# Kernel tuning notes

Hardware: AMD Instinct MI355X
Metric: run time of the kernel (lower is better)

## Reference

```python
import jax, jax.numpy as jnp
import numpy as np

N = 100000; R2 = 500; H = 200; T = 3; E = 300000; R2E = 400000
SE = 4000; SR = 8; S2E = 8000
SLOPE = (1.0 / 8 + 1.0 / 3) / 2  # eval-mode F.rrelu negative slope


def l2norm(x):
    # F.normalize(x) along dim=1 with eps=1e-12
    return x / jnp.maximum(jnp.linalg.norm(x, axis=-1, keepdims=True), 1e-12)


def rrelu(x):
    return jnp.where(x >= 0, x, x * SLOPE)


def seg_mean(vals, seg, num):
    # mean of vals rows grouped by seg id; absent groups stay zero (matches x_input init)
    s = jax.ops.segment_sum(vals, seg, num_segments=num)
    c = jax.ops.segment_sum(jnp.ones((vals.shape[0],), vals.dtype), seg, num_segments=num)
    return s / jnp.maximum(c, 1.0)[:, None]


def lstm_cell(x, h, c, Wih, Whh, bih, bhh):
    g = x @ Wih.T + bih + h @ Whh.T + bhh
    i, f, gg, o = jnp.split(g, 4, axis=1)
    c2 = jax.nn.sigmoid(f) * c + jax.nn.sigmoid(i) * jnp.tanh(gg)
    return jax.nn.sigmoid(o) * jnp.tanh(c2), c2


def gru_cell(x, h, Wih, Whh, bih, bhh):
    gi = x @ Wih.T + bih
    gh = h @ Whh.T + bhh
    ir, iz, inn = jnp.split(gi, 3, axis=1)
    hr, hz, hn = jnp.split(gh, 3, axis=1)
    r = jax.nn.sigmoid(ir + hr)
    z = jax.nn.sigmoid(iz + hz)
    n = jnp.tanh(inn + r * hn)
    return (1 - z) * n + z * h


def rgcn_layer(h, rel_emb, src, dst, et, Wn, Wloop, Wevolve, num_nodes):
    # UnionRGCNLayer: msg = (h_src + rel_emb[etype]) @ W_neighbor, sum-aggregated at dst;
    # self loop uses evolve weight for nodes with in-edges, plain loop weight otherwise.
    msg = (h[src] + rel_emb[et]) @ Wn
    agg = jax.ops.segment_sum(msg, dst, num_segments=num_nodes)
    indeg = jax.ops.segment_sum(jnp.ones((src.shape[0],), h.dtype), dst, num_segments=num_nodes)
    loop = jnp.where((indeg > 0)[:, None], h @ Wevolve, h @ Wloop)
    return rrelu(agg + loop)


def setup_inputs() -> dict:
    key = jax.random.key(0)
    ks = iter(jax.random.split(key, 48))
    s = 1.0 / np.sqrt(H)
    d = {}
    d['src'] = jax.random.randint(next(ks), (T, E), 0, N)
    d['dst'] = jax.random.randint(next(ks), (T, E), 0, N)
    d['etype'] = jax.random.randint(next(ks), (T, E), 0, R2)
    d['r_to_e'] = jax.random.randint(next(ks), (T, R2E), 0, N)
    d['r_seg'] = jax.random.randint(next(ks), (T, R2E), 0, R2)
    d['s_src'] = jax.random.randint(next(ks), (T, SE), 0, R2)
    d['s_dst'] = jax.random.randint(next(ks), (T, SE), 0, R2)
    d['s_etype'] = jax.random.randint(next(ks), (T, SE), 0, SR)
    d['s_r_to_e'] = jax.random.randint(next(ks), (T, S2E), 0, R2)
    d['s_r_seg'] = jax.random.randint(next(ks), (T, S2E), 0, SR)
    d['dynamic_emb'] = jax.random.normal(next(ks), (N, H), jnp.float32)
    d['emb_rel'] = jax.random.normal(next(ks), (R2, H), jnp.float32) * s
    d['p_rel'] = jax.random.normal(next(ks), (SR, H), jnp.float32) * s
    d['Wih1'] = jax.random.normal(next(ks), (4 * H, 2 * H), jnp.float32) * s
    d['Whh1'] = jax.random.normal(next(ks), (4 * H, H), jnp.float32) * s
    d['bih1'] = jax.random.normal(next(ks), (4 * H,), jnp.float32) * s
    d['bhh1'] = jax.random.normal(next(ks), (4 * H,), jnp.float32) * s
    d['Wih2'] = jax.random.normal(next(ks), (4 * H, 2 * H), jnp.float32) * s
    d['Whh2'] = jax.random.normal(next(ks), (4 * H, H), jnp.float32) * s
    d['bih2'] = jax.random.normal(next(ks), (4 * H,), jnp.float32) * s
    d['bhh2'] = jax.random.normal(next(ks), (4 * H,), jnp.float32) * s
    d['Wih3'] = jax.random.normal(next(ks), (3 * H, H), jnp.float32) * s
    d['Whh3'] = jax.random.normal(next(ks), (3 * H, H), jnp.float32) * s
    d['bih3'] = jax.random.normal(next(ks), (3 * H,), jnp.float32) * s
    d['bhh3'] = jax.random.normal(next(ks), (3 * H,), jnp.float32) * s
    d['Wihe'] = jax.random.normal(next(ks), (3 * H, H), jnp.float32) * s
    d['Whhe'] = jax.random.normal(next(ks), (3 * H, H), jnp.float32) * s
    d['bihe'] = jax.random.normal(next(ks), (3 * H,), jnp.float32) * s
    d['bhhe'] = jax.random.normal(next(ks), (3 * H,), jnp.float32) * s
    for nm in ('Wn', 'Wl', 'We', 'sWn', 'sWl', 'sWe'):
        d[nm] = jax.random.normal(next(ks), (2, H, H), jnp.float32) * s
    return d


def reference(src, dst, etype, r_to_e, r_seg, s_src, s_dst, s_etype, s_r_to_e, s_r_seg,
              dynamic_emb, emb_rel, p_rel,
              Wih1, Whh1, bih1, bhh1, Wih2, Whh2, bih2, bhh2,
              Wih3, Whh3, bih3, bhh3, Wihe, Whhe, bihe, bhhe,
              Wn, Wl, We, sWn, sWl, sWe):
    h = l2norm(dynamic_emb)  # layer_norm=True path
    h_0 = c_0 = p_h_0 = p_c_0 = None
    history_embs = []
    rel_embs = []
    for t in range(T):
        # per-relation mean of involved entity embeddings (r_to_e grouped by uniq_r)
        x_input = seg_mean(h[r_to_e[t]], r_seg[t], R2)
        if t == 0:
            h_prev, c_prev = emb_rel, x_input
        else:
            h_prev, c_prev = h_0, c_0
        x_cat = jnp.concatenate([emb_rel, x_input], axis=1)
        h_0, c_0 = lstm_cell(x_cat, h_prev, c_prev, Wih1, Whh1, bih1, bhh1)
        h_0 = l2norm(h_0); c_0 = l2norm(c_0)
        # super-graph: per-super-relation mean of relation embeddings
        sx = seg_mean(h_0[s_r_to_e[t]], s_r_seg[t], SR)
        if t == 0:
            ph_prev, pc_prev = p_rel, sx
        else:
            ph_prev, pc_prev = p_h_0, p_c_0
        sx_cat = jnp.concatenate([p_rel, sx], axis=1)
        p_h_0, p_c_0 = lstm_cell(sx_cat, ph_prev, pc_prev, Wih2, Whh2, bih2, bhh2)
        p_h_0 = l2norm(p_h_0); p_c_0 = l2norm(p_c_0)
        # super RGCN over relation-nodes (2 UnionRGCN layers, same rel emb per layer)
        cur = h_0
        for l in range(2):
            cur = rgcn_layer(cur, p_h_0, s_src[t], s_dst[t], s_etype[t], sWn[l], sWl[l], sWe[l], R2)
        cur = l2norm(cur)
        h_0 = gru_cell(cur, h_0, Wih3, Whh3, bih3, bhh3)
        h_0 = l2norm(h_0)
        rel_embs.append(h_0)
        # entity RGCN over the snapshot graph
        cur_h = h
        for l in range(2):
            cur_h = rgcn_layer(cur_h, h_0, src[t], dst[t], etype[t], Wn[l], Wl[l], We[l], N)
        cur_h = l2norm(cur_h)
        h = gru_cell(cur_h, h, Wihe, Whhe, bihe, bhhe)
        h = l2norm(h)
        history_embs.append(h)
    return jnp.stack(history_embs), jnp.stack(rel_embs)
```

## Files before the change

kernel.cpp:

```cpp
#include <hip/hip_runtime.h>
#include <math.h>

#define N_NODES 100000
#define H 200
#define R2 500
#define T_STEPS 3
#define E_EDGES 300000
#define R2E 400000
#define SE_EDGES 4000
#define SR 8
#define S2E 8000
#define SLOPE 0.22916666666666666f
#define NB 64
#define RCHUNK ((R2E + NB - 1) / NB)
#define NCH 128
#define CHSZ ((N_NODES + NCH - 1) / NCH)
#define SPT  ((CHSZ + 255) / 256)

typedef unsigned short u16;
typedef unsigned int u32;
typedef __bf16 bf8 __attribute__((ext_vector_type(8)));
typedef float f32x4 __attribute__((ext_vector_type(4)));

static __device__ __forceinline__ float sigf(float x) { return 1.f / (1.f + expf(-x)); }
static __device__ __forceinline__ float bf2f(u32 lo16) {
    u32 v = lo16 << 16; float f; __builtin_memcpy(&f, &v, 4); return f;
}
static __device__ __forceinline__ u16 f2bf(float a) {
    __bf16 x = (__bf16)a; u16 u; __builtin_memcpy(&u, &x, 2); return u;
}
static __device__ __forceinline__ u32 pk2(float a, float b) {
    return (u32)f2bf(a) | ((u32)f2bf(b) << 16);
}
static __device__ __forceinline__ int xcd_swz(int b, int nwg) {
    int q = nwg >> 3, r = nwg & 7;
    int xcd = b & 7, u = b >> 3;
    int start = xcd * q + (xcd < r ? xcd : r);
    return start + u;
}

__global__ __launch_bounds__(256) void l2norm_k(const float* __restrict__ src, float* __restrict__ dst,
                                                u16* __restrict__ mir, int rows) {
    int wave = threadIdx.x >> 6, lane = threadIdx.x & 63;
    int r = blockIdx.x * 4 + wave;
    if (r >= rows) return;
    float4 v = make_float4(0.f, 0.f, 0.f, 0.f);
    if (lane < 50) v = *(const float4*)(src + (size_t)r * H + lane * 4);
    float s = v.x * v.x + v.y * v.y + v.z * v.z + v.w * v.w;
    for (int o = 32; o > 0; o >>= 1) s += __shfl_down(s, o);
    float rn = 1.f / fmaxf(sqrtf(__shfl(s, 0)), 1e-12f);
    if (lane < 50) {
        float4 o4 = make_float4(v.x * rn, v.y * rn, v.z * rn, v.w * rn);
        *(float4*)(dst + (size_t)r * H + lane * 4) = o4;
        if (mir) {
            uint2 u; u.x = pk2(o4.x, o4.y); u.y = pk2(o4.z, o4.w);
            *(uint2*)(mir + (size_t)r * H + lane * 4) = u;
        }
    }
}

__global__ __launch_bounds__(256) void l2norm_b_k(u16* __restrict__ buf, int rows) {
    int wave = threadIdx.x >> 6, lane = threadIdx.x & 63;
    int r = blockIdx.x * 4 + wave;
    if (r >= rows) return;
    uint2 u = make_uint2(0, 0);
    if (lane < 50) u = *(const uint2*)(buf + (size_t)r * H + lane * 4);
    float x0 = bf2f(u.x & 0xffff), x1 = bf2f(u.x >> 16);
    float x2 = bf2f(u.y & 0xffff), x3 = bf2f(u.y >> 16);
    float s = x0 * x0 + x1 * x1 + x2 * x2 + x3 * x3;
    for (int o = 32; o > 0; o >>= 1) s += __shfl_down(s, o);
    float rn = 1.f / fmaxf(sqrtf(__shfl(s, 0)), 1e-12f);
    if (lane < 50) {
        uint2 o2; o2.x = pk2(x0 * rn, x1 * rn); o2.y = pk2(x2 * rn, x3 * rn);
        *(uint2*)(buf + (size_t)r * H + lane * 4) = o2;
    }
}

__global__ void wconv4_k(const float* __restrict__ W0, const float* __restrict__ W1,
                         const float* __restrict__ W2, const float* __restrict__ W3,
                         u16* __restrict__ o) {
    int m = blockIdx.y;
    const float* W = (m == 0) ? W0 : (m == 1) ? W1 : (m == 2) ? W2 : W3;
    int i = blockIdx.x * 256 + threadIdx.x;
    if (i < 40000) { int n = i / 200, k = i - n * 200; o[m * 40000 + i] = f2bf(W[k * 200 + n]); }
}
__global__ void wconv2_k(const float* __restrict__ Wa, const float* __restrict__ Wb, u16* __restrict__ o) {
    int i = blockIdx.x * 256 + threadIdx.x;
    if (i < 240000) o[i] = f2bf(i < 120000 ? Wa[i] : Wb[i - 120000]);
}

__global__ void cnt3_k(const int* __restrict__ d, int total, int per_t, int stride, int* __restrict__ cnt) {
    int i = blockIdx.x * 256 + threadIdx.x;
    if (i < total) { int t = i / per_t; atomicAdd(&cnt[t * stride + d[i]], 1); }
}

__global__ __launch_bounds__(256) void seg_cnt3_k(const int* __restrict__ seg, int per_t, int nseg,
                                                  int blocks_per_t, int* __restrict__ cnt) {
    __shared__ int lc[500];
    int t = blockIdx.x / blocks_per_t;
    int pb = blockIdx.x - t * blocks_per_t;
    const int* s = seg + (size_t)t * per_t;
    int* c = cnt + (size_t)t * nseg;
    for (int i = threadIdx.x; i < nseg; i += 256) lc[i] = 0;
    __syncthreads();
    int chunk = (per_t + blocks_per_t - 1) / blocks_per_t;
    int beg = pb * chunk;
    int end = beg + chunk; if (end > per_t) end = per_t;
    for (int i = beg + threadIdx.x; i < end; i += 256) atomicAdd(&lc[s[i]], 1);
    __syncthreads();
    for (int i = threadIdx.x; i < nseg; i += 256) if (lc[i]) atomicAdd(&c[i], lc[i]);
}

__global__ __launch_bounds__(256) void hist3_k(const int* __restrict__ seg,
                                               int* __restrict__ hist, int* __restrict__ cnt) {
    __shared__ int lc[R2];
    int t = blockIdx.x / NB;
    int pb = blockIdx.x - t * NB;
    const int* s = seg + (size_t)t * R2E;
    for (int i = threadIdx.x; i < R2; i += 256) lc[i] = 0;
    __syncthreads();
    int beg = pb * RCHUNK;
    int end = beg + RCHUNK; if (end > R2E) end = R2E;
    for (int i = beg + threadIdx.x; i < end; i += 256) atomicAdd(&lc[s[i]], 1);
    __syncthreads();
    int* hrow = hist + (size_t)(t * NB + pb) * R2;
    int* c = cnt + (size_t)t * R2;
    for (int i = threadIdx.x; i < R2; i += 256) {
        hrow[i] = lc[i];
        if (lc[i]) atomicAdd(&c[i], lc[i]);
    }
}

__global__ __launch_bounds__(1024) void scan3_k(const int* __restrict__ cntA, int* __restrict__ offA,
                                                int* __restrict__ curA, int n) {
    const int b = blockIdx.x;
    const int* cnt = cntA + (size_t)b * n;
    int* off = offA + (size_t)b * (n + 1);
    int* cur = curA + (size_t)b * n;
    __shared__ int part[1024];
    int tid = threadIdx.x;
    int per = (n + 1023) / 1024;
    int s0 = tid * per;
    int e0 = s0 + per; if (e0 > n) e0 = n;
    int sum = 0;
    for (int i = s0; i < e0; ++i) sum += cnt[i];
    part[tid] = sum;
    __syncthreads();
    for (int d = 1; d < 1024; d <<= 1) {
        int v = (tid >= d) ? part[tid - d] : 0;
        __syncthreads();
        part[tid] += v;
        __syncthreads();
    }
    int excl = (tid == 0) ? 0 : part[tid - 1];
    for (int i = s0; i < e0; ++i) { off[i] = excl; cur[i] = excl; excl += cnt[i]; }
    if (tid == 1023) off[n] = excl;
}

__global__ __launch_bounds__(256) void scanA_k(const int* __restrict__ cntA, int* __restrict__ bsum, int n) {
    int b = blockIdx.x;
    int t = b / NCH, ch = b - t * NCH;
    const int* cnt = cntA + (size_t)t * n;
    int base = ch * CHSZ;
    int cend = base + CHSZ; if (cend > n) cend = n;
    int s0 = base + threadIdx.x * SPT;
    int e0 = s0 + SPT; if (e0 > cend) e0 = cend;
    int sum = 0;
    for (int i = s0; i < e0 && i < cend; ++i) sum += cnt[i];
    __shared__ int red[256];
    red[threadIdx.x] = (s0 < cend) ? sum : 0;
    __syncthreads();
    for (int o = 128; o > 0; o >>= 1) {
        if (threadIdx.x < o) red[threadIdx.x] += red[threadIdx.x + o];
        __syncthreads();
    }
    if (threadIdx.x == 0) bsum[t * NCH + ch] = red[0];
}

__global__ __launch_bounds__(128) void scanB_k(const int* __restrict__ bsum, int* __restrict__ boff,
                                               int* __restrict__ offA, int n) {
    int t = blockIdx.x;
    int tid = threadIdx.x;
    __shared__ int part[128];
    int v = bsum[t * NCH + tid];
    part[tid] = v;
    __syncthreads();
    for (int d = 1; d < 128; d <<= 1) {
        int u = (tid >= d) ? part[tid - d] : 0;
        __syncthreads();
        part[tid] += u;
        __syncthreads();
    }
    boff[t * NCH + tid] = part[tid] - v;
    if (tid == 127) offA[(size_t)t * (n + 1) + n] = part[127];
}

__global__ __launch_bounds__(256) void scanC_k(const int* __restrict__ cntA, const int* __restrict__ boff,
                                               int* __restrict__ offA, int* __restrict__ curA, int n) {
    int b = blockIdx.x;
    int t = b / NCH, ch = b - t * NCH;
    const int* cnt = cntA + (size_t)t * n;
    int* off = offA + (size_t)t * (n + 1);
    int* cur = curA + (size_t)t * n;
    int base = ch * CHSZ;
    int cend = base + CHSZ; if (cend > n) cend = n;
    int s0 = base + threadIdx.x * SPT;
    int e0 = s0 + SPT; if (e0 > cend) e0 = cend;
    int sum = 0;
    for (int i = s0; i < e0 && i < cend; ++i) sum += cnt[i];
    __shared__ int part[256];
    int my = (s0 < cend) ? sum : 0;
    part[threadIdx.x] = my;
    __syncthreads();
    for (int d = 1; d < 256; d <<= 1) {
        int u = (threadIdx.x >= d) ? part[threadIdx.x - d] : 0;
        __syncthreads();
        part[threadIdx.x] += u;
        __syncthreads();
    }
    int excl = boff[t * NCH + ch] + part[threadIdx.x] - my;
    for (int i = s0; i < e0 && i < cend; ++i) {
        off[i] = excl; cur[i] = excl; excl += cnt[i];
    }
}

__global__ __launch_bounds__(64) void offs3_k(const int* __restrict__ hist, const int* __restrict__ csr,
                                              int* __restrict__ offb) {
    int b = blockIdx.x;
    int t = b / R2, s = b - t * R2;
    int lane = threadIdx.x;
    int v = hist[(size_t)(t * NB + lane) * R2 + s];
    int pre = v;
    for (int o = 1; o < 64; o <<= 1) {
        int u = __shfl_up(pre, o);
        if (lane >= o) pre += u;
    }
    int base = csr[(size_t)t * (R2 + 1) + s];
    offb[(size_t)(t * NB + lane) * R2 + s] = base + pre - v;
}

__global__ __launch_bounds__(256) void part3_k(const int* __restrict__ seg, const int* __restrict__ val,
                                               const int* __restrict__ offb, int* __restrict__ outp) {
    __shared__ int cur[R2];
    int t = blockIdx.x / NB;
    int pb = blockIdx.x - t * NB;
    const int* s = seg + (size_t)t * R2E;
    const int* v = val + (size_t)t * R2E;
    const int* ob = offb + (size_t)(t * NB + pb) * R2;
    int* o = outp + (size_t)t * R2E;
    for (int i = threadIdx.x; i < R2; i += 256) cur[i] = ob[i];
    __syncthreads();
    int beg = pb * RCHUNK;
    int end = beg + RCHUNK; if (end > R2E) end = R2E;
    for (int i = beg + threadIdx.x; i < end; i += 256) {
        int p = atomicAdd(&cur[s[i]], 1);
        o[p] = v[i];
    }
}

__global__ void scatter3_k(const int* __restrict__ dst, const int* __restrict__ src,
                           const int* __restrict__ et, int* __restrict__ cur,
                           int* __restrict__ psrc, int* __restrict__ pet,
                           int per_t, int stride, int total) {
    int i = blockIdx.x * 256 + threadIdx.x;
    if (i < total) {
        int t = i / per_t;
        int p = atomicAdd(&cur[t * stride + dst[i]], 1);
        psrc[(size_t)t * per_t + p] = src[i];
        pet[(size_t)t * per_t + p] = et[i];
    }
}
__global__ void zlist3_k(const int* __restrict__ cnt, int* __restrict__ zl, int* __restrict__ nz,
                         int n, int total) {
    int i = blockIdx.x * 256 + threadIdx.x;
    if (i < total && cnt[i] == 0) {
        int t = i / n;
        int p = atomicAdd(&nz[t], 1);
        zl[(size_t)t * n + p] = i - t * n;
    }
}

#define SEG_CW 25
__global__ __launch_bounds__(256) void seg_acc_k(const float* __restrict__ hsrc,
                                                 const int* __restrict__ idx,
                                                 const int* __restrict__ seg, int n,
                                                 float* __restrict__ acc, int nseg) {
    __shared__ float lacc[500 * SEG_CW];
    int cg = blockIdx.x & 7;
    int pb = blockIdx.x >> 3;
    int NPB = gridDim.x >> 3;
    int t = threadIdx.x;
    for (int i = t; i < nseg * SEG_CW; i += 256) lacc[i] = 0.f;
    __syncthreads();
    int chunk = (n + NPB - 1) / NPB;
    int beg = pb * chunk;
    int end = beg + chunk; if (end > n) end = n;
    if (t < 250) {
        int il = t / SEG_CW;
        int c = t - il * SEG_CW;
        int col = cg * SEG_CW + c;
        for (int i = beg + il; i < end; i += 10) {
            int r = seg[i];
            int e = idx[i];
            atomicAdd(&lacc[r * SEG_CW + c], hsrc[(size_t)e * H + col]);
        }
    }
    __syncthreads();
    for (int i = t; i < nseg * SEG_CW; i += 256) {
        int r = i / SEG_CW, c = i - (i / SEG_CW) * SEG_CW;
        atomicAdd(&acc[(size_t)r * H + cg * SEG_CW + c], lacc[i]);
    }
}

__global__ void seg_div_k(float* __restrict__ acc, const int* __restrict__ cnt, int rows) {
    int i = blockIdx.x * blockDim.x + threadIdx.x;
    if (i < rows * H) {
        int c = cnt[i / H];
        acc[i] /= (float)(c > 0 ? c : 1);
    }
}

__global__ __launch_bounds__(256) void seg_mean_part_k(const u16* __restrict__ h,
                                                       const int* __restrict__ per,
                                                       const int* __restrict__ off,
                                                       float* __restrict__ xacc, int nseg) {
    int r = blockIdx.x >> 2;
    int p = blockIdx.x & 3;
    if (r >= nseg) return;
    int wv = threadIdx.x >> 6, lane = threadIdx.x & 63;
    int beg = off[r], end = off[r + 1];
    float a0 = 0.f, a1 = 0.f, a2 = 0.f, a3 = 0.f;
    for (int i = beg + p * 4 + wv; i < end; i += 16) {
        int e = per[i];
        if (lane < 50) {
            uint2 u = ((const uint2*)(h + (size_t)e * H))[lane];
            a0 += bf2f(u.x & 0xffff); a1 += bf2f(u.x >> 16);
            a2 += bf2f(u.y & 0xffff); a3 += bf2f(u.y >> 16);
        }
    }
    __shared__ float red[4][200];
    if (lane < 50) *(float4*)(&red[wv][lane * 4]) = make_float4(a0, a1, a2, a3);
    __syncthreads();
    int t = threadIdx.x;
    if (t < 200) {
        float s = red[0][t] + red[1][t] + red[2][t] + red[3][t];
        atomicAdd(&xacc[(size_t)r * H + t], s);
    }
}
__global__ void seg_fin_k(float* __restrict__ acc, const int* __restrict__ off, int nseg) {
    int i = blockIdx.x * 256 + threadIdx.x;
    if (i < nseg * H) {
        int r = i / H;
        int c = off[r + 1] - off[r];
        acc[i] /= (float)(c > 0 ? c : 1);
    }
}

__global__ __launch_bounds__(256) void lstm_k(const float* __restrict__ x1, const float* __restrict__ x2,
                                              const float* __restrict__ hprev, const float* __restrict__ cprev,
                                              const float* __restrict__ Wih, const float* __restrict__ Whh,
                                              const float* __restrict__ bih, const float* __restrict__ bhh,
                                              float* __restrict__ hout, float* __restrict__ cout, int rows) {
    int r = blockIdx.x;
    if (r >= rows) return;
    __shared__ float xb[2 * H], hb[H], gb[4 * H], hv[H], cv[H];
    __shared__ float red[8];
    int t = threadIdx.x;
    for (int i = t; i < 2 * H; i += 256)
        xb[i] = (i < H) ? x1[(size_t)r * H + i] : x2[(size_t)r * H + i - H];
    if (t < H) hb[t] = hprev[(size_t)r * H + t];
    __syncthreads();
    for (int j = t; j < 4 * H; j += 256) {
        float s = bih[j] + bhh[j];
        const float* wi = Wih + (size_t)j * 2 * H;
        for (int k = 0; k < 2 * H; ++k) s += xb[k] * wi[k];
        const float* wh = Whh + (size_t)j * H;
        for (int k = 0; k < H; ++k) s += hb[k] * wh[k];
        gb[j] = s;
    }
    __syncthreads();
    if (t < H) {
        float ig = sigf(gb[t]);
        float fg = sigf(gb[H + t]);
        float gg = tanhf(gb[2 * H + t]);
        float og = sigf(gb[3 * H + t]);
        float c2 = fg * cprev[(size_t)r * H + t] + ig * gg;
        cv[t] = c2;
        hv[t] = og * tanhf(c2);
    }
    __syncthreads();
    float sh = 0.f, sc = 0.f;
    if (t < H) { sh = hv[t] * hv[t]; sc = cv[t] * cv[t]; }
    for (int o = 32; o > 0; o >>= 1) { sh += __shfl_down(sh, o); sc += __shfl_down(sc, o); }
    if ((t & 63) == 0) { red[t >> 6] = sh; red[4 + (t >> 6)] = sc; }
    __syncthreads();
    if (t == 0) {
        red[0] = 1.f / fmaxf(sqrtf(red[0] + red[1] + red[2] + red[3]), 1e-12f);
        red[4] = 1.f / fmaxf(sqrtf(red[4] + red[5] + red[6] + red[7]), 1e-12f);
    }
    __syncthreads();
    if (t < H) {
        hout[(size_t)r * H + t] = hv[t] * red[0];
        cout[(size_t)r * H + t] = cv[t] * red[4];
    }
}

__global__ __launch_bounds__(256) void gru_small_k(const float* __restrict__ x, const float* __restrict__ h,
                                                   const float* __restrict__ Wih, const float* __restrict__ Whh,
                                                   const float* __restrict__ bih, const float* __restrict__ bhh,
                                                   float* __restrict__ outp, u16* __restrict__ mirp, int rows) {
    int r = blockIdx.x;
    if (r >= rows) return;
    __shared__ float xb[H], hb[H], gi[3 * H], gh[3 * H], ov[H];
    __shared__ float red[4];
    int t = threadIdx.x;
    if (t < H) { xb[t] = x[(size_t)r * H + t]; hb[t] = h[(size_t)r * H + t]; }
    __syncthreads();
    for (int j = t; j < 3 * H; j += 256) {
        float si = bih[j], sh2 = bhh[j];
        const float* wi = Wih + (size_t)j * H;
        const float* wh = Whh + (size_t)j * H;
        for (int k = 0; k < H; ++k) { si += xb[k] * wi[k]; sh2 += hb[k] * wh[k]; }
        gi[j] = si; gh[j] = sh2;
    }
    __syncthreads();
    if (t < H) {
        float rr = sigf(gi[t] + gh[t]);
        float zz = sigf(gi[H + t] + gh[H + t]);
        float nn = tanhf(gi[2 * H + t] + rr * gh[2 * H + t]);
        ov[t] = (1.f - zz) * nn + zz * hb[t];
    }
    __syncthreads();
    float s = (t < H) ? ov[t] * ov[t] : 0.f;
    for (int o = 32; o > 0; o >>= 1) s += __shfl_down(s, o);
    if ((t & 63) == 0) red[t >> 6] = s;
    __syncthreads();
    if (t == 0) red[0] = 1.f / fmaxf(sqrtf(red[0] + red[1] + red[2] + red[3]), 1e-12f);
    __syncthreads();
    if (t < H) {
        float v = ov[t] * red[0];
        outp[(size_t)r * H + t] = v;
        mirp[(size_t)r * H + t] = f2bf(v);
    }
}

__global__ __launch_bounds__(256) void sup_agg_csr_k(const float* __restrict__ cur, const float* __restrict__ prel,
                                                     const int* __restrict__ soff, const int* __restrict__ sssrc,
                                                     const int* __restrict__ sset, float* __restrict__ sagg) {
    int r = blockIdx.x;
    int t = threadIdx.x;
    if (t >= H) return;
    int beg = soff[r], end = soff[r + 1];
    float acc = 0.f;
    for (int i = beg; i < end; ++i) {
        int s = sssrc[i], et = sset[i];
        acc += cur[(size_t)s * H + t] + prel[(size_t)et * H + t];
    }
    sagg[(size_t)r * H + t] = acc;
}

__global__ __launch_bounds__(256) void sup_comb_k(const float* __restrict__ agg, const float* __restrict__ cur,
                                                  const float* __restrict__ Wn, const float* __restrict__ We,
                                                  const float* __restrict__ Wl, const int* __restrict__ indeg,
                                                  float* __restrict__ outp) {
    int r = blockIdx.x;
    __shared__ float ar[H], cr[H];
    int t = threadIdx.x;
    if (t < H) { ar[t] = agg[(size_t)r * H + t]; cr[t] = cur[(size_t)r * H + t]; }
    __syncthreads();
    const float* W2 = (indeg[r] > 0) ? We : Wl;
    if (t < H) {
        float s = 0.f;
        for (int k = 0; k < H; ++k) s += ar[k] * Wn[(size_t)k * H + t] + cr[k] * W2[(size_t)k * H + t];
        outp[(size_t)r * H + t] = (s >= 0.f) ? s : s * SLOPE;
    }
}

__global__ __launch_bounds__(256) void ent_agg_b_k(const u16* __restrict__ cur, const u16* __restrict__ rel,
                                                   const int* __restrict__ eoff, const int* __restrict__ esrc,
                                                   const int* __restrict__ eet, u16* __restrict__ agg, int n) {
    int wave = threadIdx.x >> 6, lane = threadIdx.x & 63;
    int v = blockIdx.x * 4 + wave;
    if (v >= n) return;
    float a0 = 0.f, a1 = 0.f, a2 = 0.f, a3 = 0.f;
    bool act = lane < 50;
    int beg = eoff[v], end = eoff[v + 1];
    int i = beg;
    for (; i + 2 <= end; i += 2) {
        int e0 = esrc[i], t0 = eet[i];
        int e1 = esrc[i + 1], t1 = eet[i + 1];
        if (act) {
            uint2 h0 = ((const uint2*)(cur + (size_t)e0 * H))[lane];
            uint2 h1 = ((const uint2*)(cur + (size_t)e1 * H))[lane];
            uint2 r0 = ((const uint2*)(rel + (size_t)t0 * H))[lane];
            uint2 r1 = ((const uint2*)(rel + (size_t)t1 * H))[lane];
            a0 += bf2f(h0.x & 0xffff) + bf2f(r0.x & 0xffff) + bf2f(h1.x & 0xffff) + bf2f(r1.x & 0xffff);
            a1 += bf2f(h0.x >> 16) + bf2f(r0.x >> 16) + bf2f(h1.x >> 16) + bf2f(r1.x >> 16);
            a2 += bf2f(h0.y & 0xffff) + bf2f(r0.y & 0xffff) + bf2f(h1.y & 0xffff) + bf2f(r1.y & 0xffff);
            a3 += bf2f(h0.y >> 16) + bf2f(r0.y >> 16) + bf2f(h1.y >> 16) + bf2f(r1.y >> 16);
        }
    }
    if (i < end) {
        int e0 = esrc[i], t0 = eet[i];
        if (act) {
            uint2 h0 = ((const uint2*)(cur + (size_t)e0 * H))[lane];
            uint2 r0 = ((const uint2*)(rel + (size_t)t0 * H))[lane];
            a0 += bf2f(h0.x & 0xffff) + bf2f(r0.x & 0xffff);
            a1 += bf2f(h0.x >> 16) + bf2f(r0.x >> 16);
            a2 += bf2f(h0.y & 0xffff) + bf2f(r0.y & 0xffff);
            a3 += bf2f(h0.y >> 16) + bf2f(r0.y >> 16);
        }
    }
    if (act) {
        uint2 o; o.x = pk2(a0, a1); o.y = pk2(a2, a3);
        ((uint2*)(agg + (size_t)v * H))[lane] = o;
    }
}

__global__ __launch_bounds__(128) void gemm_bp_k(const u16* __restrict__ A1, const u16* __restrict__ A2,
                                                 const u16* __restrict__ B1, const u16* __restrict__ B2,
                                                 u16* __restrict__ Cm, int M, int Nc) {
    __shared__ __bf16 Bs[64 * 200];
    const int tid = threadIdx.x;
    int idx2 = xcd_swz(blockIdx.x, gridDim.x);
    const int m0 = (idx2 >> 2) * 128;
    const int n0 = (idx2 & 3) * 64;
    const int w = tid >> 6, lane = tid & 63;
    const int lr = lane & 15, lo = lane >> 4;
    const int mbase = m0 + w * 64;

    bf8 zb;
#pragma unroll
    for (int e = 0; e < 8; ++e) zb[e] = (__bf16)0.f;

    f32x4 acc[4][4];
#pragma unroll
    for (int i = 0; i < 4; ++i)
#pragma unroll
        for (int j = 0; j < 4; ++j)
#pragma unroll
            for (int e = 0; e < 4; ++e) acc[i][j][e] = 0.f;

    auto stageB = [&](const u16* Bp) {
        for (int ch = tid; ch < 1600; ch += 128) {
            int n = ch / 25, q = ch - n * 25;
            int ng = n0 + n;
            uint4 v = make_uint4(0, 0, 0, 0);
            if (ng < Nc) v = *(const uint4*)(Bp + (size_t)ng * 200 + q * 8);
            *(uint4*)(&Bs[n * 200 + q * 8]) = v;
        }
    };
    auto loadA = [&](bf8* buf, const u16* Ap, int kt7) {
        int kk = kt7 * 32 + lo * 8;
        bool kv = kk < 200;
#pragma unroll
        for (int mf = 0; mf < 4; ++mf) {
            int m = mbase + mf * 16 + lr;
            bf8 v = zb;
            if (kv && m < M) v = *(const bf8*)(Ap + (size_t)m * 200 + kk);
            buf[mf] = v;
        }
    };
    auto mmaStep = [&](bf8* a, int kt7) {
        int kk = kt7 * 32 + lo * 8;
        int kcl = (kk < 200) ? kk : 0;
#pragma unroll
        for (int nf = 0; nf < 4; ++nf) {
            bf8 b = *(const bf8*)(&Bs[(nf * 16 + lr) * 200 + kcl]);
#pragma unroll
            for (int mf = 0; mf < 4; ++mf)
                acc[mf][nf] = __builtin_amdgcn_mfma_f32_16x16x32_bf16(a[mf], b, acc[mf][nf], 0, 0, 0);
        }
    };

    bf8 a0[4], a1[4];
    stageB(B1);
    __syncthreads();
    loadA(a0, A1, 0);
#pragma unroll
    for (int kt = 0; kt < 7; ++kt) {
        if (kt < 6) loadA((kt & 1) ? a0 : a1, A1, kt + 1);
        mmaStep((kt & 1) ? a1 : a0, kt);
    }
    __syncthreads();
    stageB(B2);
    __syncthreads();
    loadA(a0, A2, 0);
#pragma unroll
    for (int kt = 0; kt < 7; ++kt) {
        if (kt < 6) loadA((kt & 1) ? a0 : a1, A2, kt + 1);
        mmaStep((kt & 1) ? a1 : a0, kt);
    }
#pragma unroll
    for (int mf = 0; mf < 4; ++mf) {
#pragma unroll
        for (int r = 0; r < 4; ++r) {
            int m = mbase + mf * 16 + lo * 4 + r;
            if (m >= M) continue;
#pragma unroll
            for (int nf = 0; nf < 4; ++nf) {
                int n = n0 + nf * 16 + lr;
                if (n >= Nc) continue;
                float v = acc[mf][nf][r];
                v = (v >= 0.f) ? v : v * SLOPE;
                Cm[(size_t)m * Nc + n] = f2bf(v);
            }
        }
    }
}

__global__ __launch_bounds__(256) void fixup_b_k(const u16* __restrict__ h, const float* __restrict__ Wl,
                                                 const int* __restrict__ zl, const int* __restrict__ nz,
                                                 u16* __restrict__ outp) {
    __shared__ float xr[H];
    int nzv = *nz;
    for (int z = blockIdx.x; z < nzv; z += gridDim.x) {
        int row = zl[z];
        if (threadIdx.x < H) xr[threadIdx.x] = bf2f(h[(size_t)row * H + threadIdx.x]);
        __syncthreads();
        if (threadIdx.x < H) {
            float s = 0.f;
            for (int k = 0; k < H; ++k) s += xr[k] * Wl[(size_t)k * H + threadIdx.x];
            outp[(size_t)row * H + threadIdx.x] = f2bf((s >= 0.f) ? s : s * SLOPE);
        }
        __syncthreads();
    }
}

#define GCG2 13
#define GTPB 3
__global__ __launch_bounds__(256, 4) void gru_wlds_k(const u16* __restrict__ Xb, const u16* __restrict__ Hb,
                                                     const float* __restrict__ Hf, const u16* __restrict__ Wb,
                                                     const float* __restrict__ bih, const float* __restrict__ bhh,
                                                     float* __restrict__ Out, int M) {
    __shared__ __bf16 Ws[6][16 * 200];
    const int tid = threadIdx.x;
    int idx2 = xcd_swz(blockIdx.x, gridDim.x);
    const int cg = idx2 % GCG2;
    const int rb = idx2 / GCG2;
    const int w = tid >> 6, lane = tid & 63;
    const int lr = lane & 15, lo = lane >> 4;
    const int c0 = cg * 16;

    for (int ch = tid; ch < 2400; ch += 256) {
        int s = ch / 400;
        int rem = ch - s * 400;
        int col = rem / 25, q = rem - (rem / 25) * 25;
        int cc = c0 + col; if (cc > 199) cc = 199;
        uint4 v = *(const uint4*)(Wb + (size_t)(s * 200 + cc) * 200 + q * 8);
        *(uint4*)(&Ws[s][col * 200 + q * 8]) = v;
    }
    __syncthreads();

    int c = c0 + lr;
    const bool cvalid = c < 200;
    const int cc = cvalid ? c : 199;
    const float b0 = bih[cc], b1 = bih[200 + cc], b2 = bih[400 + cc];
    const float b3 = bhh[cc], b4 = bhh[200 + cc], b5 = bhh[400 + cc];

    bf8 zb;
#pragma unroll
    for (int e = 0; e < 8; ++e) zb[e] = (__bf16)0.f;

    for (int tile = 0; tile < GTPB; ++tile) {
        int mbase = (rb * GTPB + tile) * 128 + w * 32;
        if (mbase >= M) break;
        int m0r = mbase + lr;      if (m0r >= M) m0r = M - 1;
        int m1r = mbase + 16 + lr; if (m1r >= M) m1r = M - 1;
        const u16* Xp0 = Xb + (size_t)m0r * 200 + lo * 8;
        const u16* Xp1 = Xb + (size_t)m1r * 200 + lo * 8;
        const u16* Hp0 = Hb + (size_t)m0r * 200 + lo * 8;
        const u16* Hp1 = Hb + (size_t)m1r * 200 + lo * 8;

        f32x4 acc[6][2];
#pragma unroll
        for (int s = 0; s < 6; ++s)
#pragma unroll
            for (int i = 0; i < 2; ++i)
#pragma unroll
                for (int e = 0; e < 4; ++e) acc[s][i][e] = 0.f;

#pragma unroll
        for (int kt = 0; kt < 7; ++kt) {
            const int koff = kt * 32;
            const bool kv = (kt < 6) || (lo == 0);
            const int kcl = kv ? (koff + lo * 8) : 0;
            bf8 xa0 = zb, xa1 = zb, ha0 = zb, ha1 = zb;
            if (kv) {
                xa0 = *(const bf8*)(Xp0 + koff);
                xa1 = *(const bf8*)(Xp1 + koff);
                ha0 = *(const bf8*)(Hp0 + koff);
                ha1 = *(const bf8*)(Hp1 + koff);
            }
#pragma unroll
            for (int s = 0; s < 6; ++s) {
                bf8 wv = *(const bf8*)(&Ws[s][lr * 200 + kcl]);
                bf8 a0f = (s < 3) ? xa0 : ha0;
                bf8 a1f = (s < 3) ? xa1 : ha1;
                acc[s][0] = __builtin_amdgcn_mfma_f32_16x16x32_bf16(a0f, wv, acc[s][0], 0, 0, 0);
                acc[s][1] = __builtin_amdgcn_mfma_f32_16x16x32_bf16(a1f, wv, acc[s][1], 0, 0, 0);
            }
        }
        if (cvalid) {
#pragma unroll
            for (int mf = 0; mf < 2; ++mf) {
#pragma unroll
                for (int r = 0; r < 4; ++r) {
                    int m = mbase + mf * 16 + lo * 4 + r;
                    if (m >= M) continue;
                    float ir = acc[0][mf][r] + b0;
                    float iz = acc[1][mf][r] + b1;
                    float in_ = acc[2][mf][r] + b2;
                    float hr = acc[3][mf][r] + b3;
                    float hz = acc[4][mf][r] + b4;
                    float hn = acc[5][mf][r] + b5;
                    float rr = sigf(ir + hr);
                    float zz = sigf(iz + hz);
                    float nn = tanhf(in_ + rr * hn);
                    Out[(size_t)m * H + c] = (1.f - zz) * nn + zz * Hf[(size_t)m * H + c];
                }
            }
        }
    }
}

extern "C" void kernel_launch(void* const* d_in, const int* in_sizes, int n_in,
                              void* d_out, int out_size, void* d_ws, size_t ws_size,
                              hipStream_t stream) {
    (void)in_sizes; (void)n_in; (void)out_size; (void)ws_size;
    const int* src  = (const int*)d_in[0];
    const int* dst  = (const int*)d_in[1];
    const int* etyp = (const int*)d_in[2];
    const int* rte  = (const int*)d_in[3];
    const int* rseg = (const int*)d_in[4];
    const int* ssrc = (const int*)d_in[5];
    const int* sdst = (const int*)d_in[6];
    const int* setp = (const int*)d_in[7];
    const int* srte = (const int*)d_in[8];
    const int* srseg= (const int*)d_in[9];
    const float* dyn     = (const float*)d_in[10];
    const float* emb_rel = (const float*)d_in[11];
    const float* p_rel   = (const float*)d_in[12];
    const float* Wih1 = (const float*)d_in[13]; const float* Whh1 = (const float*)d_in[14];
    const float* bih1 = (const float*)d_in[15]; const float* bhh1 = (const float*)d_in[16];
    const float* Wih2 = (const float*)d_in[17]; const float* Whh2 = (const float*)d_in[18];
    const float* bih2 = (const float*)d_in[19]; const float* bhh2 = (const float*)d_in[20];
    const float* Wih3 = (const float*)d_in[21]; const float* Whh3 = (const float*)d_in[22];
    const float* bih3 = (const float*)d_in[23]; const float* bhh3 = (const float*)d_in[24];
    const float* Wihe = (const float*)d_in[25]; const float* Whhe = (const float*)d_in[26];
    const float* bihe = (const float*)d_in[27]; const float* bhhe = (const float*)d_in[28];
    const float* Wn  = (const float*)d_in[29];
    const float* Wl  = (const float*)d_in[30];
    const float* We  = (const float*)d_in[31];
    const float* sWn = (const float*)d_in[32];
    const float* sWl = (const float*)d_in[33];
    const float* sWe = (const float*)d_in[34];

    float* out = (float*)d_out;
    const size_t NH = (size_t)N_NODES * H;
    float* relout = out + 3 * NH;

    char* wp = (char*)d_ws;
    auto carve = [&](size_t bytes) -> void* {
        void* p = (void*)wp;
        wp += (bytes + 255) & ~(size_t)255;
        return p;
    };
    u16* aggB = (u16*)carve(NH * 2);
    u16* m0b  = (u16*)carve(NH * 2);
    u16* m1b  = (u16*)carve(NH * 2);
    u16* hmir = (u16*)carve(NH * 2);
    u16* relm = (u16*)carve((size_t)R2 * H * 2);
    u16* wtB  = (u16*)carve((size_t)400000 * 2);
    float* h0a  = (float*)carve((size_t)R2 * H * 4);
    float* c0b  = (float*)carve((size_t)R2 * H * 4);
    float* xin  = (float*)carve((size_t)R2 * H * 4);
    float* srelA= (float*)carve((size_t)R2 * H * 4);
    float* srelB= (float*)carve((size_t)R2 * H * 4);
    float* sagg = (float*)carve((size_t)R2 * H * 4);
    float* sxin = (float*)carve((size_t)SR * H * 4);
    float* p_h  = (float*)carve((size_t)SR * H * 4);
    float* p_c  = (float*)carve((size_t)SR * H * 4);
    int* eoff3  = (int*)carve((size_t)3 * (N_NODES + 1) * 4);
    int* esrcp3 = (int*)carve((size_t)3 * E_EDGES * 4);
    int* eetp3  = (int*)carve((size_t)3 * E_EDGES * 4);
    int* zl3    = (int*)carve((size_t)3 * N_NODES * 4);
    int* nz3    = (int*)carve(3 * 4);
    int* rcsr3  = (int*)carve((size_t)3 * (R2 + 1) * 4);
    int* rper3  = (int*)carve((size_t)3 * R2E * 4);
    int* sindeg3= (int*)carve((size_t)3 * R2 * 4);
    int* scnt3  = (int*)carve((size_t)3 * SR * 4);
    int* hist3  = (int*)carve((size_t)3 * NB * R2 * 4);
    int* offb3  = (int*)carve((size_t)3 * NB * R2 * 4);
    int* soff3  = (int*)carve((size_t)3 * (R2 + 1) * 4);
    int* scur3  = (int*)carve((size_t)3 * R2 * 4);
    int* sssrc3 = (int*)carve((size_t)3 * SE_EDGES * 4);
    int* sset3  = (int*)carve((size_t)3 * SE_EDGES * 4);
    int* bsum3  = (int*)carve((size_t)3 * NCH * 4);
    int* boff3  = (int*)carve((size_t)3 * NCH * 4);
    int* ecnt3 = (int*)m0b;
    int* rcnt3 = (int*)m0b + 3 * N_NODES;
    int* ecur3 = (int*)aggB;
    int* rcur3 = (int*)aggB + 3 * N_NODES;

    dim3 wg4(157, 4);
    wconv4_k<<<wg4, 256, 0, stream>>>(Wn, We, Wn + 40000, We + 40000, wtB);
    wconv2_k<<<938, 256, 0, stream>>>(Wihe, Whhe, wtB + 160000);

    hipMemsetAsync(ecnt3, 0, (size_t)3 * N_NODES * 4, stream);
    hipMemsetAsync(rcnt3, 0, (size_t)3 * R2 * 4, stream);
    hipMemsetAsync(nz3, 0, 3 * 4, stream);
    hipMemsetAsync(sindeg3, 0, (size_t)3 * R2 * 4, stream);
    hipMemsetAsync(scnt3, 0, (size_t)3 * SR * 4, stream);
    cnt3_k<<<(3 * E_EDGES + 255) / 256, 256, 0, stream>>>(dst, 3 * E_EDGES, E_EDGES, N_NODES, ecnt3);
    scanA_k<<<3 * NCH, 256, 0, stream>>>(ecnt3, bsum3, N_NODES);
    scanB_k<<<3, 128, 0, stream>>>(bsum3, boff3, eoff3, N_NODES);
    scanC_k<<<3 * NCH, 256, 0, stream>>>(ecnt3, boff3, eoff3, ecur3, N_NODES);
    scatter3_k<<<(3 * E_EDGES + 255) / 256, 256, 0, stream>>>(dst, src, etyp, ecur3, esrcp3, eetp3,
                                                             E_EDGES, N_NODES, 3 * E_EDGES);
    zlist3_k<<<(3 * N_NODES + 255) / 256, 256, 0, stream>>>(ecnt3, zl3, nz3, N_NODES, 3 * N_NODES);
    hist3_k<<<3 * NB, 256, 0, stream>>>(rseg, hist3, rcnt3);
    scan3_k<<<3, 1024, 0, stream>>>(rcnt3, rcsr3, rcur3, R2);
    offs3_k<<<3 * R2, 64, 0, stream>>>(hist3, rcsr3, offb3);
    part3_k<<<3 * NB, 256, 0, stream>>>(rseg, rte, offb3, rper3);
    seg_cnt3_k<<<12, 256, 0, stream>>>(srseg, S2E, SR, 4, scnt3);
    cnt3_k<<<(3 * SE_EDGES + 255) / 256, 256, 0, stream>>>(sdst, 3 * SE_EDGES, SE_EDGES, R2, sindeg3);
    scan3_k<<<3, 1024, 0, stream>>>(sindeg3, soff3, scur3, R2);
    scatter3_k<<<(3 * SE_EDGES + 255) / 256, 256, 0, stream>>>(sdst, ssrc, setp, scur3, sssrc3, sset3,
                                                              SE_EDGES, R2, 3 * SE_EDGES);

    l2norm_k<<<(N_NODES + 3) / 4, 256, 0, stream>>>(dyn, out + NH, hmir, N_NODES);

    const int gw  = 4 * ((N_NODES + 127) / 128);
    const int NRB2 = (N_NODES + GTPB * 128 - 1) / (GTPB * 128);
    const int gwg = GCG2 * NRB2;

    for (int t = 0; t < T_STEPS; ++t) {
        const int* srte_t = srte + (size_t)t * S2E;
        const int* srseg_t= srseg + (size_t)t * S2E;
        const int* eoff_t = eoff3 + (size_t)t * (N_NODES + 1);
        const int* esrc_t = esrcp3 + (size_t)t * E_EDGES;
        const int* eet_t  = eetp3 + (size_t)t * E_EDGES;
        const int* zl_t   = zl3 + (size_t)t * N_NODES;
        const int* nz_t   = nz3 + t;
        const int* rcsr_t = rcsr3 + (size_t)t * (R2 + 1);
        const int* rper_t = rper3 + (size_t)t * R2E;
        const int* sind_t = sindeg3 + (size_t)t * R2;
        const int* scnt_t = scnt3 + (size_t)t * SR;
        const int* soff_t = soff3 + (size_t)t * (R2 + 1);
        const int* sssrc_t= sssrc3 + (size_t)t * SE_EDGES;
        const int* sset_t = sset3 + (size_t)t * SE_EDGES;

        float* hin  = (t == 0) ? out + NH : out + (size_t)(t - 1) * NH;
        float* hist = out + (size_t)t * NH;
        float* rel_t = relout + (size_t)t * R2 * H;
        const float* hprev = (t == 0) ? emb_rel : relout + (size_t)(t - 1) * R2 * H;
        const float* cprev = (t == 0) ? xin : c0b;
        const float* php   = (t == 0) ? p_rel : p_h;
        const float* pcp   = (t == 0) ? sxin : p_c;

        hipMemsetAsync(xin, 0, (size_t)R2 * H * 4, stream);
        seg_mean_part_k<<<R2 * 4, 256, 0, stream>>>(hmir, rper_t, rcsr_t, xin, R2);
        seg_fin_k<<<(R2 * H + 255) / 256, 256, 0, stream>>>(xin, rcsr_t, R2);
        lstm_k<<<R2, 256, 0, stream>>>(emb_rel, xin, hprev, cprev, Wih1, Whh1, bih1, bhh1, h0a, c0b, R2);
        hipMemsetAsync(sxin, 0, (size_t)SR * H * 4, stream);
        seg_acc_k<<<16 * 8, 256, 0, stream>>>(h0a, srte_t, srseg_t, S2E, sxin, SR);
        seg_div_k<<<(SR * H + 255) / 256, 256, 0, stream>>>(sxin, scnt_t, SR);
        lstm_k<<<SR, 256, 0, stream>>>(p_rel, sxin, php, pcp, Wih2, Whh2, bih2, bhh2, p_h, p_c, SR);
        sup_agg_csr_k<<<R2, 256, 0, stream>>>(h0a, p_h, soff_t, sssrc_t, sset_t, sagg);
        sup_comb_k<<<R2, 256, 0, stream>>>(sagg, h0a, sWn, sWe, sWl, sind_t, srelA);
        sup_agg_csr_k<<<R2, 256, 0, stream>>>(srelA, p_h, soff_t, sssrc_t, sset_t, sagg);
        sup_comb_k<<<R2, 256, 0, stream>>>(sagg, srelA, sWn + H * H, sWe + H * H, sWl + H * H, sind_t, srelB);
        l2norm_k<<<(R2 + 3) / 4, 256, 0, stream>>>(srelB, srelB, (u16*)nullptr, R2);
        gru_small_k<<<R2, 256, 0, stream>>>(srelB, h0a, Wih3, Whh3, bih3, bhh3, rel_t, relm, R2);

        ent_agg_b_k<<<(N_NODES + 3) / 4, 256, 0, stream>>>(hmir, relm, eoff_t, esrc_t, eet_t, aggB, N_NODES);
        gemm_bp_k<<<gw, 128, 0, stream>>>(aggB, hmir, wtB, wtB + 40000, m0b, N_NODES, H);
        fixup_b_k<<<2048, 256, 0, stream>>>(hmir, Wl, zl_t, nz_t, m0b);
        ent_agg_b_k<<<(N_NODES + 3) / 4, 256, 0, stream>>>(m0b, relm, eoff_t, esrc_t, eet_t, aggB, N_NODES);
        gemm_bp_k<<<gw, 128, 0, stream>>>(aggB, m0b, wtB + 80000, wtB + 120000, m1b, N_NODES, H);
        fixup_b_k<<<2048, 256, 0, stream>>>(m0b, Wl + H * H, zl_t, nz_t, m1b);
        l2norm_b_k<<<(N_NODES + 3) / 4, 256, 0, stream>>>(m1b, N_NODES);

        gru_wlds_k<<<gwg, 256, 0, stream>>>(m1b, hmir, hin, wtB + 160000, bihe, bhhe, hist, N_NODES);
        l2norm_k<<<(N_NODES + 3) / 4, 256, 0, stream>>>(hist, hist, hmir, N_NODES);
    }
}
```

Before: 2.933 ms.

## Pad LDS strides, split B staging, bf16 GRU output, fast sigmoid/tanh

Several unrelated changes land together. The GEMM stages B in two K-halves with a padded LDS stride, and the GRU weight LDS stride is padded to 204; both aim to cut bank conflicts and LDS footprint so more blocks fit. The entity GRU now reads the previous hidden state from the bf16 mirror and writes a bf16 intermediate, which a new kernel normalizes into both fp32 and bf16 outputs, reducing fp32 traffic. Sigmoid and tanh switch to __expf-based versions, trading some accuracy for speed, and the GRU output is now rounded to bf16 before normalization.

```diff
diff --git a/kernel.cpp b/kernel.cpp
--- a/kernel.cpp
+++ b/kernel.cpp
@@ -22,7 +22,12 @@
 typedef __bf16 bf8 __attribute__((ext_vector_type(8)));
 typedef float f32x4 __attribute__((ext_vector_type(4)));
 
-static __device__ __forceinline__ float sigf(float x) { return 1.f / (1.f + expf(-x)); }
+static __device__ __forceinline__ float fsig(float x) { return 1.f / (1.f + __expf(-x)); }
+static __device__ __forceinline__ float ftanh(float x) {
+    float e = __expf(-2.f * fabsf(x));
+    float t = (1.f - e) / (1.f + e);
+    return (x >= 0.f) ? t : -t;
+}
 static __device__ __forceinline__ float bf2f(u32 lo16) {
     u32 v = lo16 << 16; float f; __builtin_memcpy(&f, &v, 4); return f;
 }
@@ -76,6 +81,26 @@
     }
 }
 
+__global__ __launch_bounds__(256) void l2norm_bb_k(const u16* __restrict__ src, float* __restrict__ dst,
+                                                   u16* __restrict__ mir, int rows) {
+    int wave = threadIdx.x >> 6, lane = threadIdx.x & 63;
+    int r = blockIdx.x * 4 + wave;
+    if (r >= rows) return;
+    uint2 u = make_uint2(0, 0);
+    if (lane < 50) u = *(const uint2*)(src + (size_t)r * H + lane * 4);
+    float x0 = bf2f(u.x & 0xffff), x1 = bf2f(u.x >> 16);
+    float x2 = bf2f(u.y & 0xffff), x3 = bf2f(u.y >> 16);
+    float s = x0 * x0 + x1 * x1 + x2 * x2 + x3 * x3;
+    for (int o = 32; o > 0; o >>= 1) s += __shfl_down(s, o);
+    float rn = 1.f / fmaxf(sqrtf(__shfl(s, 0)), 1e-12f);
+    if (lane < 50) {
+        float4 o4 = make_float4(x0 * rn, x1 * rn, x2 * rn, x3 * rn);
+        *(float4*)(dst + (size_t)r * H + lane * 4) = o4;
+        uint2 o2; o2.x = pk2(o4.x, o4.y); o2.y = pk2(o4.z, o4.w);
+        *(uint2*)(mir + (size_t)r * H + lane * 4) = o2;
+    }
+}
+
 __global__ void wconv4_k(const float* __restrict__ W0, const float* __restrict__ W1,
                          const float* __restrict__ W2, const float* __restrict__ W3,
                          u16* __restrict__ o) {
@@ -380,13 +405,13 @@
     }
     __syncthreads();
     if (t < H) {
-        float ig = sigf(gb[t]);
-        float fg = sigf(gb[H + t]);
-        float gg = tanhf(gb[2 * H + t]);
-        float og = sigf(gb[3 * H + t]);
+        float ig = fsig(gb[t]);
+        float fg = fsig(gb[H + t]);
+        float gg = ftanh(gb[2 * H + t]);
+        float og = fsig(gb[3 * H + t]);
         float c2 = fg * cprev[(size_t)r * H + t] + ig * gg;
         cv[t] = c2;
-        hv[t] = og * tanhf(c2);
+        hv[t] = og * ftanh(c2);
     }
     __syncthreads();
     float sh = 0.f, sc = 0.f;
@@ -425,9 +450,9 @@
     }
     __syncthreads();
     if (t < H) {
-        float rr = sigf(gi[t] + gh[t]);
-        float zz = sigf(gi[H + t] + gh[H + t]);
-        float nn = tanhf(gi[2 * H + t] + rr * gh[2 * H + t]);
+        float rr = fsig(gi[t] + gh[t]);
+        float zz = fsig(gi[H + t] + gh[H + t]);
+        float nn = ftanh(gi[2 * H + t] + rr * gh[2 * H + t]);
         ov[t] = (1.f - zz) * nn + zz * hb[t];
     }
     __syncthreads();
@@ -517,10 +542,11 @@
     }
 }
 
+#define BSTR 108
 __global__ __launch_bounds__(128) void gemm_bp_k(const u16* __restrict__ A1, const u16* __restrict__ A2,
                                                  const u16* __restrict__ B1, const u16* __restrict__ B2,
                                                  u16* __restrict__ Cm, int M, int Nc) {
-    __shared__ __bf16 Bs[64 * 200];
+    __shared__ __bf16 Bs[64 * BSTR];
     const int tid = threadIdx.x;
     int idx2 = xcd_swz(blockIdx.x, gridDim.x);
     const int m0 = (idx2 >> 2) * 128;
@@ -541,13 +567,13 @@
 #pragma unroll
             for (int e = 0; e < 4; ++e) acc[i][j][e] = 0.f;
 
-    auto stageB = [&](const u16* Bp) {
-        for (int ch = tid; ch < 1600; ch += 128) {
-            int n = ch / 25, q = ch - n * 25;
+    auto stageB = [&](const u16* Bp, int kbase, int nch) {
+        for (int ch = tid; ch < 64 * nch; ch += 128) {
+            int n = ch / nch, q = ch - n * nch;
             int ng = n0 + n;
             uint4 v = make_uint4(0, 0, 0, 0);
-            if (ng < Nc) v = *(const uint4*)(Bp + (size_t)ng * 200 + q * 8);
-            *(uint4*)(&Bs[n * 200 + q * 8]) = v;
+            if (ng < Nc) v = *(const uint4*)(Bp + (size_t)ng * 200 + kbase + q * 8);
+            *(uint4*)(&Bs[n * BSTR + q * 8]) = v;
         }
     };
     auto loadA = [&](bf8* buf, const u16* Ap, int kt7) {
@@ -561,12 +587,12 @@
             buf[mf] = v;
         }
     };
-    auto mmaStep = [&](bf8* a, int kt7) {
+    auto mmaStep = [&](bf8* a, int kt7, int kbase) {
         int kk = kt7 * 32 + lo * 8;
-        int kcl = (kk < 200) ? kk : 0;
+        int kcl = (kk < 200) ? (kk - kbase) : 0;
 #pragma unroll
         for (int nf = 0; nf < 4; ++nf) {
-            bf8 b = *(const bf8*)(&Bs[(nf * 16 + lr) * 200 + kcl]);
+            bf8 b = *(const bf8*)(&Bs[(nf * 16 + lr) * BSTR + kcl]);
 #pragma unroll
             for (int mf = 0; mf < 4; ++mf)
                 acc[mf][nf] = __builtin_amdgcn_mfma_f32_16x16x32_bf16(a[mf], b, acc[mf][nf], 0, 0, 0);
@@ -574,23 +600,33 @@
     };
 
     bf8 a0[4], a1[4];
-    stageB(B1);
+    stageB(B1, 0, 12);
     __syncthreads();
     loadA(a0, A1, 0);
-#pragma unroll
-    for (int kt = 0; kt < 7; ++kt) {
-        if (kt < 6) loadA((kt & 1) ? a0 : a1, A1, kt + 1);
-        mmaStep((kt & 1) ? a1 : a0, kt);
-    }
-    __syncthreads();
-    stageB(B2);
-    __syncthreads();
-    loadA(a0, A2, 0);
-#pragma unroll
-    for (int kt = 0; kt < 7; ++kt) {
-        if (kt < 6) loadA((kt & 1) ? a0 : a1, A2, kt + 1);
-        mmaStep((kt & 1) ? a1 : a0, kt);
-    }
+    loadA(a1, A1, 1); mmaStep(a0, 0, 0);
+    loadA(a0, A1, 2); mmaStep(a1, 1, 0);
+    loadA(a1, A1, 3); mmaStep(a0, 2, 0);
+    __syncthreads();
+    stageB(B1, 96, 13);
+    __syncthreads();
+    loadA(a0, A1, 4); mmaStep(a1, 3, 96);
+    loadA(a1, A1, 5); mmaStep(a0, 4, 96);
+    loadA(a0, A1, 6); mmaStep(a1, 5, 96);
+    loadA(a1, A2, 0); mmaStep(a0, 6, 96);
+    __syncthreads();
+    stageB(B2, 0, 12);
+    __syncthreads();
+    loadA(a0, A2, 1); mmaStep(a1, 0, 0);
+    loadA(a1, A2, 2); mmaStep(a0, 1, 0);
+    loadA(a0, A2, 3); mmaStep(a1, 2, 0);
+    __syncthreads();
+    stageB(B2, 96, 13);
+    __syncthreads();
+    loadA(a1, A2, 4); mmaStep(a0, 3, 96);
+    loadA(a0, A2, 5); mmaStep(a1, 4, 96);
+    loadA(a1, A2, 6); mmaStep(a0, 5, 96);
+    mmaStep(a1, 6, 96);
+
 #pragma unroll
     for (int mf = 0; mf < 4; ++mf) {
 #pragma unroll
@@ -629,11 +665,12 @@
 
 #define GCG2 13
 #define GTPB 3
+#define WSTR 204
 __global__ __launch_bounds__(256, 4) void gru_wlds_k(const u16* __restrict__ Xb, const u16* __restrict__ Hb,
-                                                     const float* __restrict__ Hf, const u16* __restrict__ Wb,
+                                                     const u16* __restrict__ Wb,
                                                      const float* __restrict__ bih, const float* __restrict__ bhh,
-                                                     float* __restrict__ Out, int M) {
-    __shared__ __bf16 Ws[6][16 * 200];
+                                                     u16* __restrict__ Outb, int M) {
+    __shared__ __bf16 Ws[6][16 * WSTR];
     const int tid = threadIdx.x;
     int idx2 = xcd_swz(blockIdx.x, gridDim.x);
     const int cg = idx2 % GCG2;
@@ -648,7 +685,7 @@
         int col = rem / 25, q = rem - (rem / 25) * 25;
         int cc = c0 + col; if (cc > 199) cc = 199;
         uint4 v = *(const uint4*)(Wb + (size_t)(s * 200 + cc) * 200 + q * 8);
-        *(uint4*)(&Ws[s][col * 200 + q * 8]) = v;
+        *(uint4*)(&Ws[s][col * WSTR + q * 8]) = v;
     }
     __syncthreads();
 
@@ -694,7 +731,7 @@
             }
 #pragma unroll
             for (int s = 0; s < 6; ++s) {
-                bf8 wv = *(const bf8*)(&Ws[s][lr * 200 + kcl]);
+                bf8 wv = *(const bf8*)(&Ws[s][lr * WSTR + kcl]);
                 bf8 a0f = (s < 3) ? xa0 : ha0;
                 bf8 a1f = (s < 3) ? xa1 : ha1;
                 acc[s][0] = __builtin_amdgcn_mfma_f32_16x16x32_bf16(a0f, wv, acc[s][0], 0, 0, 0);
@@ -714,10 +751,11 @@
                     float hr = acc[3][mf][r] + b3;
                     float hz = acc[4][mf][r] + b4;
                     float hn = acc[5][mf][r] + b5;
-                    float rr = sigf(ir + hr);
-                    float zz = sigf(iz + hz);
-                    float nn = tanhf(in_ + rr * hn);
-                    Out[(size_t)m * H + c] = (1.f - zz) * nn + zz * Hf[(size_t)m * H + c];
+                    float rr = fsig(ir + hr);
+                    float zz = fsig(iz + hz);
+                    float nn = ftanh(in_ + rr * hn);
+                    float hvv = bf2f(Hb[(size_t)m * 200 + c]);
+                    Outb[(size_t)m * 200 + c] = f2bf((1.f - zz) * nn + zz * hvv);
                 }
             }
         }
@@ -770,6 +808,7 @@
     u16* m0b  = (u16*)carve(NH * 2);
     u16* m1b  = (u16*)carve(NH * 2);
     u16* hmir = (u16*)carve(NH * 2);
+    u16* gob  = (u16*)carve(NH * 2);
     u16* relm = (u16*)carve((size_t)R2 * H * 2);
     u16* wtB  = (u16*)carve((size_t)400000 * 2);
     float* h0a  = (float*)carve((size_t)R2 * H * 4);
@@ -851,7 +890,6 @@
         const int* sssrc_t= sssrc3 + (size_t)t * SE_EDGES;
         const int* sset_t = sset3 + (size_t)t * SE_EDGES;
 
-        float* hin  = (t == 0) ? out + NH : out + (size_t)(t - 1) * NH;
         float* hist = out + (size_t)t * NH;
         float* rel_t = relout + (size_t)t * R2 * H;
         const float* hprev = (t == 0) ? emb_rel : relout + (size_t)(t - 1) * R2 * H;
@@ -882,7 +920,7 @@
         fixup_b_k<<<2048, 256, 0, stream>>>(m0b, Wl + H * H, zl_t, nz_t, m1b);
         l2norm_b_k<<<(N_NODES + 3) / 4, 256, 0, stream>>>(m1b, N_NODES);
 
-        gru_wlds_k<<<gwg, 256, 0, stream>>>(m1b, hmir, hin, wtB + 160000, bihe, bhhe, hist, N_NODES);
-        l2norm_k<<<(N_NODES + 3) / 4, 256, 0, stream>>>(hist, hist, hmir, N_NODES);
-    }
-}
+        gru_wlds_k<<<gwg, 256, 0, stream>>>(m1b, hmir, wtB + 160000, bihe, bhhe, gob, N_NODES);
+        l2norm_bb_k<<<(N_NODES + 3) / 4, 256, 0, stream>>>(gob, hist, hmir, N_NODES);
+    }
+}
```

Measured after the change: 2.826 ms. 3.7% less time.
